# Optimization experiments

Measured on AMD Instinct MI355X. Metric: run time of the kernel, lower is better.

The kernel has to match this reference:

```python
import jax, jax.numpy as jnp
import numpy as np
import math

B, N, D, KA, H = 8, 1024, 512, 16, 8
QD = D // 4
HD = D // H


def qsplit(x):
    q = x.shape[-1] // 4
    return x[..., :q], x[..., q:2*q], x[..., 2*q:3*q], x[..., 3*q:]


def hprod(p, q):
    pr, pi, pj, pk = qsplit(p)
    qr, qi, qj, qk = qsplit(q)
    return jnp.concatenate([
        pr*qr - pi*qi - pj*qj - pk*qk,
        pr*qi + pi*qr + pj*qk - pk*qj,
        pr*qj - pi*qk + pj*qr + pk*qi,
        pr*qk + pi*qj - pj*qi + pk*qr,
    ], axis=-1)


def qconj(x):
    r, i, j, k = qsplit(x)
    return jnp.concatenate([r, -i, -j, -k], axis=-1)


def qlin(x, w, b):
    # w: [4, qo, qi] -> Hamilton block matrix [4qo, 4qi]
    r, i, j, k = w[0], w[1], w[2], w[3]
    W = jnp.concatenate([
        jnp.concatenate([r, -i, -j, -k], axis=1),
        jnp.concatenate([i,  r, -k,  j], axis=1),
        jnp.concatenate([j,  k,  r, -i], axis=1),
        jnp.concatenate([k, -j,  i,  r], axis=1),
    ], axis=0)
    return x @ W.T + b


def qln(x, gamma, beta):
    # per-component LayerNorm over Q; gamma/beta: [4, Q]
    qd = x.shape[-1] // 4
    xs = x.reshape(x.shape[:-1] + (4, qd))
    m = xs.mean(-1, keepdims=True)
    v = xs.var(-1, keepdims=True)
    y = (xs - m) / jnp.sqrt(v + 1e-5) * gamma + beta
    return y.reshape(x.shape)


def setup_inputs():
    key = jax.random.key(0)
    ks = jax.random.split(key, 20)
    lim = math.sqrt(6.0 / (2 * QD))  # xavier for [QD, QD]
    def qw(k):
        return jax.random.uniform(k, (4, QD, QD), minval=-lim, maxval=lim)
    return {
        'q': jax.random.normal(ks[0], (B, N, D), dtype=jnp.float32),
        'spike': jax.random.uniform(ks[1], (B, N), dtype=jnp.float32),
        'mask': jnp.ones((B, N), dtype=jnp.float32),
        'theta_logit': jnp.float32(0.0),
        'w_prim': qw(ks[2]), 'b_prim': jnp.zeros((D,), jnp.float32),
        'anchors': jax.random.normal(ks[3], (KA, D)) * 0.5,
        'log_sigma': jnp.zeros((KA,), jnp.float32),
        'w_aggr': qw(ks[4]), 'b_aggr': jnp.zeros((D,), jnp.float32),
        'w_q': qw(ks[5]), 'b_q': jnp.zeros((D,), jnp.float32),
        'w_k': qw(ks[6]), 'b_k': jnp.zeros((D,), jnp.float32),
        'w_v': qw(ks[7]), 'b_v': jnp.zeros((D,), jnp.float32),
        'w_o': qw(ks[8]), 'b_o': jnp.zeros((D,), jnp.float32),
        'ln_gamma': jnp.ones((4, QD), jnp.float32),
        'ln_beta': jnp.zeros((4, QD), jnp.float32),
    }


def reference(q, spike, mask, theta_logit, w_prim, b_prim, anchors, log_sigma,
              w_aggr, b_aggr, w_q, b_q, w_k, b_k, w_v, b_v, w_o, b_o,
              ln_gamma, ln_beta):
    b, n, d = q.shape
    qd = d // 4
    # --- SpikeQuaternionRotation: rotate toward K-axis by theta = theta_max*spike ---
    theta_max = (jnp.pi / 2) * jax.nn.sigmoid(theta_logit)
    theta = theta_max * spike                      # [B, N]
    c = jnp.cos(theta)[..., None]
    s = jnp.sin(theta)[..., None]
    z = jnp.zeros_like(c)
    rot = jnp.concatenate([
        jnp.broadcast_to(c, (b, n, qd)),
        jnp.broadcast_to(z, (b, n, qd)),
        jnp.broadcast_to(z, (b, n, qd)),
        jnp.broadcast_to(s, (b, n, qd)),
    ], axis=-1)
    q_rot = hprod(rot, q)                          # [B, N, D]

    # --- PrimaryLayer: per-cell quaternion transform ---
    msg_p = qlin(q_rot, w_prim, b_prim)

    # --- QuaternionAnchorLayer ---
    a_conj = qconj(anchors)                        # [KA, D]
    prod = hprod(q_rot[:, None, :, :], a_conj[None, :, None, :])  # [B, KA, N, D]
    dist = jnp.sum(prod * prod, axis=-1)           # [B, KA, N]
    sigma_sq = jnp.maximum(jnp.exp(log_sigma) ** 2, 1e-6)
    incid = jnp.exp(-dist / sigma_sq[None, :, None]) * mask[:, None, :]
    denom = jnp.maximum(incid.sum(-1, keepdims=True), 1e-6)
    h = jnp.einsum('bkn,bnd->bkd', incid, q_rot) / denom  # [B, KA, D]
    h = qlin(h, w_aggr, b_aggr)

    # --- QuaternionMHA(query=q_rot, key=h, value=h), no mask ---
    Qh = qlin(q_rot, w_q, b_q).reshape(b, n, H, HD)
    Kh = qlin(h, w_k, b_k).reshape(b, KA, H, HD)
    Vh = qlin(h, w_v, b_v).reshape(b, KA, H, HD)
    scores = jnp.einsum('bqhd,bkhd->bhqk', Qh, Kh) / jnp.sqrt(jnp.float32(HD))
    attn = jax.nn.softmax(scores, axis=-1)
    out = jnp.einsum('bhqk,bkhd->bqhd', attn, Vh).reshape(b, n, d)
    msg_a = qlin(out, w_o, b_o)

    # --- residual + per-component LayerNorm ---
    return qln(q + msg_p + msg_a, ln_gamma, ln_beta)
```

## Files before the change

kernel.cpp:

```cpp
#include <hip/hip_runtime.h>
#include <hip/hip_bf16.h>

typedef __hip_bfloat16 bf16;
typedef __attribute__((ext_vector_type(8))) short bf16x8;
typedef __attribute__((ext_vector_type(4))) float f32x4;

__device__ __forceinline__ float bflo(unsigned u) { return __uint_as_float(u << 16); }
__device__ __forceinline__ float bfhi(unsigned u) { return __uint_as_float(u & 0xffff0000u); }
__device__ __forceinline__ bool probe_f32(const void* mask) {
  return *(const unsigned*)mask == 0x3F800000u;
}
__device__ __forceinline__ float ldin(const void* p, size_t i, bool f32) {
  return f32 ? ((const float*)p)[i] : (float)((const bf16*)p)[i];
}


__global__ __launch_bounds__(256) void prologue(
    const void* w0, const void* w1, const void* w2, const void* w3,
    const void* w4, const void* w5,
    const void* b0, const void* b1, const void* b2, const void* b3,
    const void* b4, const void* b5, const void* g_, const void* be,
    const void* q, const void* spike, const void* theta_logit, const void* mask,
    bf16* __restrict__ Wall, float* __restrict__ biasF,
    bf16* __restrict__ q_rot, float* __restrict__ qn) {
  bool f32 = probe_f32(mask);
  int blk = blockIdx.x, t = threadIdx.x;
  if (blk < 1536) {
    int E = blk * 1024 + t * 4;
    int g = E >> 9;
    int wi = g >> 9;
    int o = g & 511;
    int k0 = E & 511;
    const void* src = wi == 0 ? w0 : wi == 1 ? w1 : wi == 2 ? w2 : wi == 3 ? w3 : wi == 4 ? w4 : w5;
    int ro = o >> 7, a = o & 127, co = k0 >> 7;
    int comp = ro ^ co;
    float sgn = ((0x284Eu >> (ro * 4 + co)) & 1u) ? -1.0f : 1.0f;
    bf16 ov[4];
    #pragma unroll
    for (int j = 0; j < 4; ++j) {
      int b2 = (k0 & 127) + j;
      ov[j] = (bf16)(ldin(src, comp * 16384 + a * 128 + b2, f32) * sgn);
    }
    int r = g & 63, c = k0 >> 3;
    size_t off = (size_t)(g >> 6) * 65536 + (size_t)((c >> 2) * 4096 + (r >> 4) * 1024
               + ((c & 3) * 16 + (r & 15)) * 16 + (k0 & 7) * 2);
    *(uint2*)((char*)Wall + off) = *(const uint2*)ov;
  } else if (blk < 1544) {
    int b = blk - 1536;
    const void* src = b == 0 ? b0 : b == 1 ? b1 : b == 2 ? b2 : b == 3 ? b3
                    : b == 4 ? b4 : b == 5 ? b5 : b == 6 ? g_ : be;
    biasF[b * 512 + t] = ldin(src, t, f32);
    biasF[b * 512 + 256 + t] = ldin(src, 256 + t, f32);
  } else {
    int row = (blk - 1544) * 2 + (t >> 7);
    int l = t & 127;
    float tl = ldin(theta_logit, 0, f32);
    float tmax = 1.5707963267948966f / (1.0f + __expf(-tl));
    float th = tmax * ldin(spike, row, f32);
    float c = cosf(th), s = sinf(th);
    size_t base = (size_t)row * 512;
    float a = ldin(q, base + l, f32), b = ldin(q, base + 128 + l, f32);
    float cc = ldin(q, base + 256 + l, f32), d = ldin(q, base + 384 + l, f32);
    float r0 = c * a - s * d;
    float r1 = c * b - s * cc;
    float r2 = c * cc + s * b;
    float r3 = c * d + s * a;
    bf16* orow = q_rot + base;
    orow[l] = (bf16)r0; orow[128 + l] = (bf16)r1; orow[256 + l] = (bf16)r2; orow[384 + l] = (bf16)r3;
    qn[(size_t)row * 128 + l] = r0 * r0 + r1 * r1 + r2 * r2 + r3 * r3;
  }
}

__device__ __forceinline__ void stage_B64(const bf16* __restrict__ Bw, int n0, char* Bs, int t) {
  const char* src = (const char*)Bw + (size_t)(n0 >> 6) * 65536;
  #pragma unroll
  for (int i = 0; i < 16; ++i)
    *(uint4*)(Bs + t * 16 + i * 4096) = *(const uint4*)(src + t * 16 + i * 4096);
}

__global__ __launch_bounds__(256, 2) void gemm_dist(
    const bf16* __restrict__ A, const bf16* __restrict__ Bw,
    const float* __restrict__ bias0, const float* __restrict__ bias1,
    bf16* __restrict__ MQ,
    const float* __restrict__ qn, const void* anchors, const void* lsig,
    const void* mask, float* __restrict__ h_part, float* __restrict__ pd_part) {
  __shared__ char smem[77952];
  const int t = threadIdx.x;
  if (blockIdx.x >= 128) {
    char* Bs = smem;
    const int g = blockIdx.x - 128;
    const int wave = t >> 6, lane = t & 63;
    const int quad = lane >> 4, l16 = lane & 15;
    const int m0 = (g & 31) * 256, n0 = (g >> 5) * 64;
    stage_B64(Bw, n0, Bs, t);
    __syncthreads();
    const int mbase = m0 + wave * 64;
    f32x4 acc[4][4] = {};
    bf16x8 areg[2][4], breg[2][4];
    #pragma unroll
    for (int mt = 0; mt < 4; ++mt)
      areg[0][mt] = *(const bf16x8*)(A + (size_t)(mbase + mt * 16 + l16) * 512 + quad * 8);
    #pragma unroll
    for (int nt = 0; nt < 4; ++nt)
      breg[0][nt] = *(const bf16x8*)(Bs + nt * 1024 + lane * 16);
    #pragma unroll
    for (int kk = 0; kk < 16; ++kk) {
      const int cur = kk & 1, nxt = cur ^ 1;
      if (kk < 15) {
        const int k2 = (kk + 1) * 32;
        #pragma unroll
        for (int mt = 0; mt < 4; ++mt)
          areg[nxt][mt] = *(const bf16x8*)(A + (size_t)(mbase + mt * 16 + l16) * 512 + k2 + quad * 8);
        #pragma unroll
        for (int nt = 0; nt < 4; ++nt)
          breg[nxt][nt] = *(const bf16x8*)(Bs + (kk + 1) * 4096 + nt * 1024 + lane * 16);
      }
      #pragma unroll
      for (int mt = 0; mt < 4; ++mt)
        #pragma unroll
        for (int nt = 0; nt < 4; ++nt)
          acc[mt][nt] = __builtin_amdgcn_mfma_f32_16x16x32_bf16(areg[cur][mt], breg[cur][nt],
                                                                acc[mt][nt], 0, 0, 0);
    }
    #pragma unroll
    for (int nt = 0; nt < 4; ++nt) {
      int col = n0 + nt * 16 + l16;
      float bv = col < 512 ? bias0[col] : bias1[col - 512];
      #pragma unroll
      for (int mt = 0; mt < 4; ++mt) {
        int rb = mbase + mt * 16 + quad * 4;
        #pragma unroll
        for (int r = 0; r < 4; ++r)
          MQ[(size_t)(rb + r) * 1024 + col] = (bf16)(acc[mt][nt][r] + bv);
      }
    }
  } else {
    bool f32 = probe_f32(mask);
    bf16*  qr    = (bf16*)smem;
    float* an    = (float*)(smem + 65536);
    float* sIncT = (float*)(smem + 73728);
    float* rs    = (float*)(smem + 77824);
    float* pd    = (float*)(smem + 77888);
    int bb = blockIdx.x;
    int b = bb >> 4, nc = bb & 15;
    {
      const uint4* src = (const uint4*)((const bf16*)A + ((size_t)b * 1024 + nc * 64) * 512);
      uint4* dst = (uint4*)qr;
      #pragma unroll
      for (int i = 0; i < 16; ++i) dst[t + i * 256] = src[t + i * 256];
    }
    for (int i = t; i < 2048; i += 256) {
      int k = i >> 7, l = i & 127;
      float a0 = ldin(anchors, k * 512 + l, f32);
      float a1 = ldin(anchors, k * 512 + 128 + l, f32);
      float a2 = ldin(anchors, k * 512 + 256 + l, f32);
      float a3 = ldin(anchors, k * 512 + 384 + l, f32);
      an[i] = a0 * a0 + a1 * a1 + a2 * a2 + a3 * a3;
    }
    if (t < 16) {
      float ls = ldin(lsig, t, f32);
      float ssq = __expf(ls); ssq = fmaxf(ssq * ssq, 1e-6f);
      rs[t] = -1.0f / ssq;
      pd[t] = 0.0f;
    }
    __syncthreads();
    {
      int rl = t >> 2, part = t & 3;
      int n = nc * 64 + rl;
      const float* qrow = qn + ((size_t)b * 1024 + n) * 128 + part * 32;
      f32x4 q4[8];
      #pragma unroll
      for (int i = 0; i < 8; ++i) q4[i] = *(const f32x4*)(qrow + i * 4);
      float sc[16] = {};
      #pragma unroll
      for (int i = 0; i < 8; ++i) {
        #pragma unroll
        for (int k = 0; k < 16; ++k) {
          f32x4 av = *(const f32x4*)(an + k * 128 + part * 32 + i * 4);
          sc[k] += q4[i][0] * av[0] + q4[i][1] * av[1] + q4[i][2] * av[2] + q4[i][3] * av[3];
        }
      }
      #pragma unroll
      for (int k = 0; k < 16; ++k) {
        sc[k] += __shfl_xor(sc[k], 1, 64);
        sc[k] += __shfl_xor(sc[k], 2, 64);
      }
      if (part == 0) {
        float mval = ldin(mask, b * 1024 + n, f32);
        #pragma unroll
        for (int k = 0; k < 16; ++k) {
          float inc = __expf(sc[k] * rs[k]) * mval;
          sIncT[rl * 16 + k] = inc;
          atomicAdd(&pd[k], inc);
        }
      }
    }
    __syncthreads();
    {
      float acc0[16] = {}, acc1[16] = {};
      for (int nn = 0; nn < 64; ++nn) {
        unsigned u = *(const unsigned*)(qr + nn * 512 + 2 * t);
        float v0 = bflo(u);
        float v1 = bfhi(u);
        f32x4 p0 = *(const f32x4*)(sIncT + nn * 16);
        f32x4 p1 = *(const f32x4*)(sIncT + nn * 16 + 4);
        f32x4 p2 = *(const f32x4*)(sIncT + nn * 16 + 8);
        f32x4 p3 = *(const f32x4*)(sIncT + nn * 16 + 12);
        #pragma unroll
        for (int j = 0; j < 4; ++j) {
          acc0[j]      += p0[j] * v0; acc1[j]      += p0[j] * v1;
          acc0[4 + j]  += p1[j] * v0; acc1[4 + j]  += p1[j] * v1;
          acc0[8 + j]  += p2[j] * v0; acc1[8 + j]  += p2[j] * v1;
          acc0[12 + j] += p3[j] * v0; acc1[12 + j] += p3[j] * v1;
        }
      }
      #pragma unroll
      for (int k = 0; k < 16; ++k) {
        size_t base = ((size_t)(b * 16 + k) * 16 + nc) * 512;
        float2 o2 = {acc0[k], acc1[k]};
        *(float2*)(h_part + base + 2 * t) = o2;
      }
    }
    if (t < 16) pd_part[((size_t)(b * 16 + t)) * 16 + nc] = pd[t];
  }
}

__device__ __forceinline__ float dotW4(const char* WallB, int gRow, const float* xp512, int c4lo) {
  const char* p = WallB + (size_t)(gRow >> 6) * 65536
                + (size_t)(((gRow >> 4) & 3) * 1024 + (gRow & 15) * 16);
  float acc = 0.0f;
  #pragma unroll
  for (int c4 = c4lo; c4 < c4lo + 4; ++c4) {
    #pragma unroll
    for (int cl = 0; cl < 4; ++cl) {
      uint4 u = *(const uint4*)(p + c4 * 4096 + cl * 256);
      const float* xp = xp512 + c4 * 32 + cl * 8;
      acc += xp[0] * bflo(u.x) + xp[1] * bfhi(u.x)
           + xp[2] * bflo(u.y) + xp[3] * bfhi(u.y)
           + xp[4] * bflo(u.z) + xp[5] * bfhi(u.z)
           + xp[6] * bflo(u.w) + xp[7] * bfhi(u.w);
    }
  }
  return acc;
}

__global__ __launch_bounds__(256) void aggr_k(
    const float* __restrict__ h_part, const float* __restrict__ pd_part,
    const bf16* __restrict__ Wall, const float* __restrict__ biasF,
    float* __restrict__ h_aggr) {
  __shared__ float xs[512];
  const char* WallB = (const char*)Wall;
  const float* ba = biasF + 1536;
  const int gy = blockIdx.x >> 7, row = blockIdx.x & 127;
  const int t = threadIdx.x;
  float dsum = 0.0f;
  #pragma unroll
  for (int nc = 0; nc < 16; ++nc) dsum += pd_part[row * 16 + nc];
  float dinv = 1.0f / fmaxf(dsum, 1e-6f);
  #pragma unroll
  for (int j = 0; j < 2; ++j) {
    int d = j * 256 + t;
    float hv = 0.0f;
    #pragma unroll
    for (int nc = 0; nc < 16; ++nc) hv += h_part[(size_t)row * 8192 + nc * 512 + d];
    xs[d] = hv * dinv;
  }
  __syncthreads();
  const int o = gy * 64 + (t >> 2), part = t & 3;
  float acc = dotW4(WallB, 1536 + o, xs, part * 4);
  acc += __shfl_xor(acc, 1, 64);
  acc += __shfl_xor(acc, 2, 64);
  if (part == 0) h_aggr[(size_t)row * 512 + o] = acc + ba[o];
}

__global__ __launch_bounds__(256) void kv_k(
    const float* __restrict__ h_aggr, const bf16* __restrict__ Wall,
    const float* __restrict__ biasF,
    float* __restrict__ Kh, float* __restrict__ Vh) {
  __shared__ float ys[512];
  const char* WallB = (const char*)Wall;
  const float* bk = biasF + 2048;
  const float* bv = biasF + 2560;
  const int gy = blockIdx.x >> 7, row = blockIdx.x & 127;
  const int t = threadIdx.x;
  #pragma unroll
  for (int j = 0; j < 2; ++j) {
    int d = j * 256 + t;
    ys[d] = h_aggr[(size_t)row * 512 + d];
  }
  __syncthreads();
  const int o = gy * 64 + (t >> 2), part = t & 3;
  float ak = dotW4(WallB, 2048 + o, ys, part * 4);
  float av = dotW4(WallB, 2560 + o, ys, part * 4);
  ak += __shfl_xor(ak, 1, 64);
  ak += __shfl_xor(ak, 2, 64);
  av += __shfl_xor(av, 1, 64);
  av += __shfl_xor(av, 2, 64);
  if (part == 0) {
    Kh[(size_t)row * 512 + o] = ak + bk[o];
    Vh[(size_t)row * 512 + o] = av + bv[o];
  }
}

__global__ __launch_bounds__(256, 2) void attn_tail(
    const bf16* __restrict__ MQ, const float* __restrict__ Kh_g,
    const float* __restrict__ Vh_g, const bf16* __restrict__ Wall,
    const float* __restrict__ biasF, const void* q, const void* mask, void* out) {
  __shared__ float KV[8 * 1092];
  __shared__ float P[16 * 132];
  const bool f32 = probe_f32(mask);
  const int t = threadIdx.x;
  const int rowbase = blockIdx.x * 16;
  const int b = rowbase >> 10;
  for (int i = t; i < 8192; i += 256) {
    int k = i >> 9, d = i & 511, h = d >> 6, dd = d & 63;
    KV[h * 1092 + k * 68 + dd] = Kh_g[(size_t)b * 8192 + i];
  }
  __syncthreads();
  {
    const int r = t >> 4, h = (t >> 1) & 7, hf = t & 1;
    const int grow = rowbase + r;
    const uint4* qp = (const uint4*)(MQ + (size_t)grow * 1024 + 512 + h * 64 + hf * 32);
    float qv[32];
    #pragma unroll
    for (int i = 0; i < 4; ++i) {
      uint4 u = qp[i];
      qv[i * 8 + 0] = bflo(u.x); qv[i * 8 + 1] = bfhi(u.x);
      qv[i * 8 + 2] = bflo(u.y); qv[i * 8 + 3] = bfhi(u.y);
      qv[i * 8 + 4] = bflo(u.z); qv[i * 8 + 5] = bfhi(u.z);
      qv[i * 8 + 6] = bflo(u.w); qv[i * 8 + 7] = bfhi(u.w);
    }
    float sc[16];
    #pragma unroll
    for (int k = 0; k < 16; ++k) {
      float s = 0.0f;
      #pragma unroll
      for (int d4 = 0; d4 < 8; ++d4) {
        f32x4 kv = *(const f32x4*)(KV + h * 1092 + k * 68 + hf * 32 + d4 * 4);
        s += qv[d4 * 4 + 0] * kv[0] + qv[d4 * 4 + 1] * kv[1]
           + qv[d4 * 4 + 2] * kv[2] + qv[d4 * 4 + 3] * kv[3];
      }
      sc[k] = s;
    }
    #pragma unroll
    for (int k = 0; k < 16; ++k) sc[k] += __shfl_xor(sc[k], 1, 64);
    if (hf == 0) {
      #pragma unroll
      for (int k = 0; k < 16; ++k) sc[k] *= 0.125f;
      float m = sc[0];
      #pragma unroll
      for (int k = 1; k < 16; ++k) m = fmaxf(m, sc[k]);
      float ssum = 0.0f;
      #pragma unroll
      for (int k = 0; k < 16; ++k) { sc[k] = __expf(sc[k] - m); ssum += sc[k]; }
      float inv = 1.0f / ssum;
      #pragma unroll
      for (int k = 0; k < 16; ++k) P[r * 132 + h * 16 + k] = sc[k] * inv;
    }
  }
  __syncthreads();
  for (int i = t; i < 8192; i += 256) {
    int k = i >> 9, d = i & 511, h = d >> 6, dd = d & 63;
    KV[h * 1092 + k * 68 + dd] = Vh_g[(size_t)b * 8192 + i];
  }
  __syncthreads();
  float pv[8][4];
  {
    const int r = t >> 4, dg = t & 15;
    #pragma unroll
    for (int h = 0; h < 8; ++h) {
      float a0 = 0, a1 = 0, a2 = 0, a3 = 0;
      #pragma unroll
      for (int k = 0; k < 16; ++k) {
        float p = P[r * 132 + h * 16 + k];
        f32x4 va = *(const f32x4*)(KV + h * 1092 + k * 68 + dg * 4);
        a0 += p * va[0]; a1 += p * va[1]; a2 += p * va[2]; a3 += p * va[3];
      }
      pv[h][0] = a0; pv[h][1] = a1; pv[h][2] = a2; pv[h][3] = a3;
    }
  }
  __syncthreads();
  char* A_lds = (char*)KV;
  {
    const int r = t >> 4, dg = t & 15;
    #pragma unroll
    for (int h = 0; h < 8; ++h) {
      int c0 = h * 64 + dg * 4;
      int off = (c0 >> 5) * 1024 + ((c0 >> 3) & 3) * 256 + r * 16 + (c0 & 7) * 2;
      bf16 ov[4] = {(bf16)pv[h][0], (bf16)pv[h][1], (bf16)pv[h][2], (bf16)pv[h][3]};
      *(uint2*)(A_lds + off) = *(const uint2*)ov;
    }
  }
  __syncthreads();
  const int wave = t >> 6, lane = t & 63, quad = lane >> 4, l16 = lane & 15;
  const char* WallB = (const char*)Wall;
  f32x4 acc[8] = {};
  bf16x8 breg[2][8];
  bf16x8 areg[2];
  areg[0] = *(const bf16x8*)(A_lds + quad * 256 + l16 * 16);
  #pragma unroll
  for (int nt = 0; nt < 8; ++nt) {
    size_t cb = (size_t)(16 + wave * 2 + (nt >> 2)) * 65536;
    breg[0][nt] = *(const bf16x8*)(WallB + cb + (nt & 3) * 1024 + lane * 16);
  }
  #pragma unroll
  for (int kk = 0; kk < 16; ++kk) {
    const int cur = kk & 1, nxt = cur ^ 1;
    if (kk < 15) {
      areg[nxt] = *(const bf16x8*)(A_lds + (kk + 1) * 1024 + quad * 256 + l16 * 16);
      #pragma unroll
      for (int nt = 0; nt < 8; ++nt) {
        size_t cb = (size_t)(16 + wave * 2 + (nt >> 2)) * 65536;
        breg[nxt][nt] = *(const bf16x8*)(WallB + cb + (kk + 1) * 4096 + (nt & 3) * 1024 + lane * 16);
      }
    }
    #pragma unroll
    for (int nt = 0; nt < 8; ++nt)
      acc[nt] = __builtin_amdgcn_mfma_f32_16x16x32_bf16(areg[cur], breg[cur][nt], acc[nt], 0, 0, 0);
  }
  const float* biasO = biasF + 1024;
  const float* gamF = biasF + 3072;
  float xv[8][4];
  float s[4] = {0, 0, 0, 0}, s2[4] = {0, 0, 0, 0};
  #pragma unroll
  for (int nt = 0; nt < 8; ++nt) {
    int gcol = wave * 128 + nt * 16 + l16;
    float bo = biasO[gcol];
    #pragma unroll
    for (int reg = 0; reg < 4; ++reg) {
      int grow = rowbase + quad * 4 + reg;
      float qv = ldin(q, (size_t)grow * 512 + gcol, f32);
      float mp = (float)MQ[(size_t)grow * 1024 + gcol];
      float x = qv + mp + acc[nt][reg] + bo;
      xv[nt][reg] = x;
      s[reg] += x; s2[reg] += x * x;
    }
  }
  #pragma unroll
  for (int reg = 0; reg < 4; ++reg) {
    #pragma unroll
    for (int off = 1; off <= 8; off <<= 1) {
      s[reg]  += __shfl_xor(s[reg], off, 64);
      s2[reg] += __shfl_xor(s2[reg], off, 64);
    }
  }
  #pragma unroll
  for (int reg = 0; reg < 4; ++reg) {
    float m = s[reg] * (1.0f / 128.0f);
    float rinv = rsqrtf(s2[reg] * (1.0f / 128.0f) - m * m + 1e-5f);
    int grow = rowbase + quad * 4 + reg;
    #pragma unroll
    for (int nt = 0; nt < 8; ++nt) {
      int gcol = wave * 128 + nt * 16 + l16;
      float y = (xv[nt][reg] - m) * rinv * gamF[gcol] + gamF[512 + gcol];
      if (f32) ((float*)out)[(size_t)grow * 512 + gcol] = y;
      else     ((bf16*)out)[(size_t)grow * 512 + gcol] = (bf16)y;
    }
  }
}

extern "C" void kernel_launch(void* const* d_in, const int* in_sizes, int n_in,
                              void* d_out, int out_size, void* d_ws, size_t ws_size,
                              hipStream_t stream) {
  (void)in_sizes; (void)n_in; (void)out_size; (void)ws_size;
  const void* q      = d_in[0];
  const void* spike  = d_in[1];
  const void* mask   = d_in[2];
  const void* tl     = d_in[3];
  const void* w_prim = d_in[4];
  const void* b_prim = d_in[5];
  const void* anchors= d_in[6];
  const void* lsig   = d_in[7];
  const void* w_aggr = d_in[8];
  const void* b_aggr = d_in[9];
  const void* w_q    = d_in[10];
  const void* b_q    = d_in[11];
  const void* w_k    = d_in[12];
  const void* b_k    = d_in[13];
  const void* w_v    = d_in[14];
  const void* b_v    = d_in[15];
  const void* w_o    = d_in[16];
  const void* b_o    = d_in[17];
  const void* gam    = d_in[18];
  const void* bet    = d_in[19];

  char* ws = (char*)d_ws;
  bf16*  Wall   = (bf16*)(ws + 0);
  bf16*  q_rot  = (bf16*)(ws + 3145728);
  float* qn     = (float*)(ws + 11534336);
  bf16*  MQ     = (bf16*)(ws + 15728640);
  float* h_part = (float*)(ws + 32505856);
  float* pd_part= (float*)(ws + 36700160);
  float* Kh     = (float*)(ws + 36708352);
  float* Vh     = (float*)(ws + 36970496);
  float* biasF  = (float*)(ws + 37232640);
  float* h_aggr = (float*)(ws + 37249024);

  prologue<<<5640, 256, 0, stream>>>(w_prim, w_q, w_o, w_aggr, w_k, w_v,
                                     b_prim, b_q, b_o, b_aggr, b_k, b_v, gam, bet,
                                     q, spike, tl, mask, Wall, biasF, q_rot, qn);
  gemm_dist<<<640, 256, 0, stream>>>(q_rot, Wall, biasF + 0, biasF + 512, MQ,
                                     qn, anchors, lsig, mask, h_part, pd_part);
  aggr_k<<<1024, 256, 0, stream>>>(h_part, pd_part, Wall, biasF, h_aggr);
  kv_k<<<1024, 256, 0, stream>>>(h_aggr, Wall, biasF, Kh, Vh);
  attn_tail<<<512, 256, 0, stream>>>(MQ, Kh, Vh, Wall, biasF, q, mask, d_out);
}
```

Baseline: 189.0 us.

## Fuse aggregation and K/V projections into one kernel; widen attention tail tiles

Merges aggr_k and kv_k into a single 1024-thread kernel per (batch, anchor) row that keeps h_aggr in shared memory, removing one launch and a global round trip. The attention tail now processes 32 rows per block instead of 16, with one thread per (row, head) and two MFMA M-tiles per wave, so K/V staging and weight loads are amortized over twice the rows. In exchange the fused kernel runs only 128 blocks, leaving much of the GPU idle and re-reading the weights per row, and the tail uses more registers and launches half as many blocks.

```diff
diff --git a/kernel.cpp b/kernel.cpp
--- a/kernel.cpp
+++ b/kernel.cpp
@@ -225,12 +225,12 @@
   }
 }
 
-__device__ __forceinline__ float dotW4(const char* WallB, int gRow, const float* xp512, int c4lo) {
+__device__ __forceinline__ float dotW8(const char* WallB, int gRow, const float* xp512, int c4lo) {
   const char* p = WallB + (size_t)(gRow >> 6) * 65536
                 + (size_t)(((gRow >> 4) & 3) * 1024 + (gRow & 15) * 16);
   float acc = 0.0f;
   #pragma unroll
-  for (int c4 = c4lo; c4 < c4lo + 4; ++c4) {
+  for (int c4 = c4lo; c4 < c4lo + 8; ++c4) {
     #pragma unroll
     for (int cl = 0; cl < 4; ++cl) {
       uint4 u = *(const uint4*)(p + c4 * 4096 + cl * 256);
@@ -244,61 +244,45 @@
   return acc;
 }
 
-__global__ __launch_bounds__(256) void aggr_k(
+__global__ __launch_bounds__(1024) void akv_k(
     const float* __restrict__ h_part, const float* __restrict__ pd_part,
     const bf16* __restrict__ Wall, const float* __restrict__ biasF,
-    float* __restrict__ h_aggr) {
+    float* __restrict__ Kh, float* __restrict__ Vh) {
   __shared__ float xs[512];
+  __shared__ float ys[512];
   const char* WallB = (const char*)Wall;
   const float* ba = biasF + 1536;
-  const int gy = blockIdx.x >> 7, row = blockIdx.x & 127;
+  const float* bk = biasF + 2048;
+  const float* bv = biasF + 2560;
+  const int row = blockIdx.x;
   const int t = threadIdx.x;
   float dsum = 0.0f;
   #pragma unroll
   for (int nc = 0; nc < 16; ++nc) dsum += pd_part[row * 16 + nc];
   float dinv = 1.0f / fmaxf(dsum, 1e-6f);
-  #pragma unroll
-  for (int j = 0; j < 2; ++j) {
-    int d = j * 256 + t;
+  if (t < 512) {
     float hv = 0.0f;
     #pragma unroll
-    for (int nc = 0; nc < 16; ++nc) hv += h_part[(size_t)row * 8192 + nc * 512 + d];
-    xs[d] = hv * dinv;
-  }
-  __syncthreads();
-  const int o = gy * 64 + (t >> 2), part = t & 3;
-  float acc = dotW4(WallB, 1536 + o, xs, part * 4);
-  acc += __shfl_xor(acc, 1, 64);
-  acc += __shfl_xor(acc, 2, 64);
-  if (part == 0) h_aggr[(size_t)row * 512 + o] = acc + ba[o];
-}
-
-__global__ __launch_bounds__(256) void kv_k(
-    const float* __restrict__ h_aggr, const bf16* __restrict__ Wall,
-    const float* __restrict__ biasF,
-    float* __restrict__ Kh, float* __restrict__ Vh) {
-  __shared__ float ys[512];
-  const char* WallB = (const char*)Wall;
-  const float* bk = biasF + 2048;
-  const float* bv = biasF + 2560;
-  const int gy = blockIdx.x >> 7, row = blockIdx.x & 127;
-  const int t = threadIdx.x;
-  #pragma unroll
-  for (int j = 0; j < 2; ++j) {
-    int d = j * 256 + t;
-    ys[d] = h_aggr[(size_t)row * 512 + d];
-  }
-  __syncthreads();
-  const int o = gy * 64 + (t >> 2), part = t & 3;
-  float ak = dotW4(WallB, 2048 + o, ys, part * 4);
-  float av = dotW4(WallB, 2560 + o, ys, part * 4);
-  ak += __shfl_xor(ak, 1, 64);
-  ak += __shfl_xor(ak, 2, 64);
-  av += __shfl_xor(av, 1, 64);
-  av += __shfl_xor(av, 2, 64);
-  if (part == 0) {
-    Kh[(size_t)row * 512 + o] = ak + bk[o];
-    Vh[(size_t)row * 512 + o] = av + bv[o];
+    for (int nc = 0; nc < 16; ++nc) hv += h_part[(size_t)row * 8192 + nc * 512 + t];
+    xs[t] = hv * dinv;
+  }
+  __syncthreads();
+  const int o = t >> 1, part = t & 1;
+  {
+    float acc = dotW8(WallB, 1536 + o, xs, part * 8);
+    acc += __shfl_xor(acc, 1, 64);
+    if (part == 0) ys[o] = acc + ba[o];
+  }
+  __syncthreads();
+  {
+    float ak = dotW8(WallB, 2048 + o, ys, part * 8);
+    float av = dotW8(WallB, 2560 + o, ys, part * 8);
+    ak += __shfl_xor(ak, 1, 64);
+    av += __shfl_xor(av, 1, 64);
+    if (part == 0) {
+      Kh[(size_t)row * 512 + o] = ak + bk[o];
+      Vh[(size_t)row * 512 + o] = av + bv[o];
+    }
   }
 }
 
@@ -307,10 +291,10 @@
     const float* __restrict__ Vh_g, const bf16* __restrict__ Wall,
     const float* __restrict__ biasF, const void* q, const void* mask, void* out) {
   __shared__ float KV[8 * 1092];
-  __shared__ float P[16 * 132];
+  __shared__ float P[32 * 132];
   const bool f32 = probe_f32(mask);
   const int t = threadIdx.x;
-  const int rowbase = blockIdx.x * 16;
+  const int rowbase = blockIdx.x * 32;
   const int b = rowbase >> 10;
   for (int i = t; i < 8192; i += 256) {
     int k = i >> 9, d = i & 511, h = d >> 6, dd = d & 63;
@@ -318,45 +302,42 @@
   }
   __syncthreads();
   {
-    const int r = t >> 4, h = (t >> 1) & 7, hf = t & 1;
+    const int r = t >> 3, h = t & 7;
     const int grow = rowbase + r;
-    const uint4* qp = (const uint4*)(MQ + (size_t)grow * 1024 + 512 + h * 64 + hf * 32);
-    float qv[32];
-    #pragma unroll
-    for (int i = 0; i < 4; ++i) {
-      uint4 u = qp[i];
-      qv[i * 8 + 0] = bflo(u.x); qv[i * 8 + 1] = bfhi(u.x);
-      qv[i * 8 + 2] = bflo(u.y); qv[i * 8 + 3] = bfhi(u.y);
-      qv[i * 8 + 4] = bflo(u.z); qv[i * 8 + 5] = bfhi(u.z);
-      qv[i * 8 + 6] = bflo(u.w); qv[i * 8 + 7] = bfhi(u.w);
-    }
-    float sc[16];
-    #pragma unroll
-    for (int k = 0; k < 16; ++k) {
-      float s = 0.0f;
-      #pragma unroll
-      for (int d4 = 0; d4 < 8; ++d4) {
-        f32x4 kv = *(const f32x4*)(KV + h * 1092 + k * 68 + hf * 32 + d4 * 4);
-        s += qv[d4 * 4 + 0] * kv[0] + qv[d4 * 4 + 1] * kv[1]
-           + qv[d4 * 4 + 2] * kv[2] + qv[d4 * 4 + 3] * kv[3];
-      }
-      sc[k] = s;
-    }
-    #pragma unroll
-    for (int k = 0; k < 16; ++k) sc[k] += __shfl_xor(sc[k], 1, 64);
-    if (hf == 0) {
-      #pragma unroll
-      for (int k = 0; k < 16; ++k) sc[k] *= 0.125f;
-      float m = sc[0];
-      #pragma unroll
-      for (int k = 1; k < 16; ++k) m = fmaxf(m, sc[k]);
-      float ssum = 0.0f;
-      #pragma unroll
-      for (int k = 0; k < 16; ++k) { sc[k] = __expf(sc[k] - m); ssum += sc[k]; }
-      float inv = 1.0f / ssum;
-      #pragma unroll
-      for (int k = 0; k < 16; ++k) P[r * 132 + h * 16 + k] = sc[k] * inv;
-    }
+    const uint4* qp = (const uint4*)(MQ + (size_t)grow * 1024 + 512 + h * 64);
+    float sc[16] = {};
+    #pragma unroll
+    for (int c = 0; c < 4; ++c) {
+      uint4 u0 = qp[c * 2], u1 = qp[c * 2 + 1];
+      float qv[16];
+      qv[0] = bflo(u0.x); qv[1] = bfhi(u0.x); qv[2] = bflo(u0.y); qv[3] = bfhi(u0.y);
+      qv[4] = bflo(u0.z); qv[5] = bfhi(u0.z); qv[6] = bflo(u0.w); qv[7] = bfhi(u0.w);
+      qv[8] = bflo(u1.x); qv[9] = bfhi(u1.x); qv[10] = bflo(u1.y); qv[11] = bfhi(u1.y);
+      qv[12] = bflo(u1.z); qv[13] = bfhi(u1.z); qv[14] = bflo(u1.w); qv[15] = bfhi(u1.w);
+      #pragma unroll
+      for (int k = 0; k < 16; ++k) {
+        const float* kp = KV + h * 1092 + k * 68 + c * 16;
+        f32x4 k0 = *(const f32x4*)(kp);
+        f32x4 k1 = *(const f32x4*)(kp + 4);
+        f32x4 k2 = *(const f32x4*)(kp + 8);
+        f32x4 k3 = *(const f32x4*)(kp + 12);
+        sc[k] += qv[0] * k0[0] + qv[1] * k0[1] + qv[2] * k0[2] + qv[3] * k0[3]
+               + qv[4] * k1[0] + qv[5] * k1[1] + qv[6] * k1[2] + qv[7] * k1[3]
+               + qv[8] * k2[0] + qv[9] * k2[1] + qv[10] * k2[2] + qv[11] * k2[3]
+               + qv[12] * k3[0] + qv[13] * k3[1] + qv[14] * k3[2] + qv[15] * k3[3];
+      }
+    }
+    #pragma unroll
+    for (int k = 0; k < 16; ++k) sc[k] *= 0.125f;
+    float m = sc[0];
+    #pragma unroll
+    for (int k = 1; k < 16; ++k) m = fmaxf(m, sc[k]);
+    float ssum = 0.0f;
+    #pragma unroll
+    for (int k = 0; k < 16; ++k) { sc[k] = __expf(sc[k] - m); ssum += sc[k]; }
+    float inv = 1.0f / ssum;
+    #pragma unroll
+    for (int k = 0; k < 16; ++k) P[r * 132 + h * 16 + k] = sc[k] * inv;
   }
   __syncthreads();
   for (int i = t; i < 8192; i += 256) {
@@ -364,40 +345,48 @@
     KV[h * 1092 + k * 68 + dd] = Vh_g[(size_t)b * 8192 + i];
   }
   __syncthreads();
-  float pv[8][4];
+  float pv[8][8];
   {
-    const int r = t >> 4, dg = t & 15;
+    const int r = t >> 3, dg = t & 7;
     #pragma unroll
     for (int h = 0; h < 8; ++h) {
-      float a0 = 0, a1 = 0, a2 = 0, a3 = 0;
+      float a0 = 0, a1 = 0, a2 = 0, a3 = 0, a4 = 0, a5 = 0, a6 = 0, a7 = 0;
       #pragma unroll
       for (int k = 0; k < 16; ++k) {
         float p = P[r * 132 + h * 16 + k];
-        f32x4 va = *(const f32x4*)(KV + h * 1092 + k * 68 + dg * 4);
-        a0 += p * va[0]; a1 += p * va[1]; a2 += p * va[2]; a3 += p * va[3];
+        const float* vp = KV + h * 1092 + k * 68 + dg * 8;
+        f32x4 v0 = *(const f32x4*)vp;
+        f32x4 v1 = *(const f32x4*)(vp + 4);
+        a0 += p * v0[0]; a1 += p * v0[1]; a2 += p * v0[2]; a3 += p * v0[3];
+        a4 += p * v1[0]; a5 += p * v1[1]; a6 += p * v1[2]; a7 += p * v1[3];
       }
       pv[h][0] = a0; pv[h][1] = a1; pv[h][2] = a2; pv[h][3] = a3;
+      pv[h][4] = a4; pv[h][5] = a5; pv[h][6] = a6; pv[h][7] = a7;
     }
   }
   __syncthreads();
   char* A_lds = (char*)KV;
   {
-    const int r = t >> 4, dg = t & 15;
+    const int r = t >> 3, dg = t & 7;
     #pragma unroll
     for (int h = 0; h < 8; ++h) {
-      int c0 = h * 64 + dg * 4;
-      int off = (c0 >> 5) * 1024 + ((c0 >> 3) & 3) * 256 + r * 16 + (c0 & 7) * 2;
-      bf16 ov[4] = {(bf16)pv[h][0], (bf16)pv[h][1], (bf16)pv[h][2], (bf16)pv[h][3]};
-      *(uint2*)(A_lds + off) = *(const uint2*)ov;
+      int c = h * 8 + dg;
+      int off = (c >> 2) * 2048 + (r >> 4) * 1024 + ((c & 3) * 16 + (r & 15)) * 16;
+      bf16 ov[8];
+      #pragma unroll
+      for (int j = 0; j < 8; ++j) ov[j] = (bf16)pv[h][j];
+      *(uint4*)(A_lds + off) = *(const uint4*)ov;
     }
   }
   __syncthreads();
   const int wave = t >> 6, lane = t & 63, quad = lane >> 4, l16 = lane & 15;
   const char* WallB = (const char*)Wall;
-  f32x4 acc[8] = {};
+  f32x4 acc[2][8] = {};
   bf16x8 breg[2][8];
-  bf16x8 areg[2];
-  areg[0] = *(const bf16x8*)(A_lds + quad * 256 + l16 * 16);
+  bf16x8 areg[2][2];
+  #pragma unroll
+  for (int mt = 0; mt < 2; ++mt)
+    areg[0][mt] = *(const bf16x8*)(A_lds + mt * 1024 + lane * 16);
   #pragma unroll
   for (int nt = 0; nt < 8; ++nt) {
     size_t cb = (size_t)(16 + wave * 2 + (nt >> 2)) * 65536;
@@ -407,7 +396,9 @@
   for (int kk = 0; kk < 16; ++kk) {
     const int cur = kk & 1, nxt = cur ^ 1;
     if (kk < 15) {
-      areg[nxt] = *(const bf16x8*)(A_lds + (kk + 1) * 1024 + quad * 256 + l16 * 16);
+      #pragma unroll
+      for (int mt = 0; mt < 2; ++mt)
+        areg[nxt][mt] = *(const bf16x8*)(A_lds + (kk + 1) * 2048 + mt * 1024 + lane * 16);
       #pragma unroll
       for (int nt = 0; nt < 8; ++nt) {
         size_t cb = (size_t)(16 + wave * 2 + (nt >> 2)) * 65536;
@@ -415,48 +406,56 @@
       }
     }
     #pragma unroll
-    for (int nt = 0; nt < 8; ++nt)
-      acc[nt] = __builtin_amdgcn_mfma_f32_16x16x32_bf16(areg[cur], breg[cur][nt], acc[nt], 0, 0, 0);
+    for (int mt = 0; mt < 2; ++mt)
+      #pragma unroll
+      for (int nt = 0; nt < 8; ++nt)
+        acc[mt][nt] = __builtin_amdgcn_mfma_f32_16x16x32_bf16(areg[cur][mt], breg[cur][nt],
+                                                              acc[mt][nt], 0, 0, 0);
   }
   const float* biasO = biasF + 1024;
   const float* gamF = biasF + 3072;
-  float xv[8][4];
-  float s[4] = {0, 0, 0, 0}, s2[4] = {0, 0, 0, 0};
-  #pragma unroll
-  for (int nt = 0; nt < 8; ++nt) {
-    int gcol = wave * 128 + nt * 16 + l16;
-    float bo = biasO[gcol];
-    #pragma unroll
-    for (int reg = 0; reg < 4; ++reg) {
-      int grow = rowbase + quad * 4 + reg;
-      float qv = ldin(q, (size_t)grow * 512 + gcol, f32);
-      float mp = (float)MQ[(size_t)grow * 1024 + gcol];
-      float x = qv + mp + acc[nt][reg] + bo;
-      xv[nt][reg] = x;
-      s[reg] += x; s2[reg] += x * x;
-    }
-  }
-  #pragma unroll
-  for (int reg = 0; reg < 4; ++reg) {
-    #pragma unroll
-    for (int off = 1; off <= 8; off <<= 1) {
-      s[reg]  += __shfl_xor(s[reg], off, 64);
-      s2[reg] += __shfl_xor(s2[reg], off, 64);
-    }
-  }
-  #pragma unroll
-  for (int reg = 0; reg < 4; ++reg) {
-    float m = s[reg] * (1.0f / 128.0f);
-    float rinv = rsqrtf(s2[reg] * (1.0f / 128.0f) - m * m + 1e-5f);
-    int grow = rowbase + quad * 4 + reg;
+  float s[2][4] = {}, s2[2][4] = {};
+  #pragma unroll
+  for (int mt = 0; mt < 2; ++mt)
     #pragma unroll
     for (int nt = 0; nt < 8; ++nt) {
       int gcol = wave * 128 + nt * 16 + l16;
-      float y = (xv[nt][reg] - m) * rinv * gamF[gcol] + gamF[512 + gcol];
-      if (f32) ((float*)out)[(size_t)grow * 512 + gcol] = y;
-      else     ((bf16*)out)[(size_t)grow * 512 + gcol] = (bf16)y;
-    }
-  }
+      float bo = biasO[gcol];
+      #pragma unroll
+      for (int reg = 0; reg < 4; ++reg) {
+        int grow = rowbase + mt * 16 + quad * 4 + reg;
+        float qv = ldin(q, (size_t)grow * 512 + gcol, f32);
+        float mp = (float)MQ[(size_t)grow * 1024 + gcol];
+        float x = qv + mp + acc[mt][nt][reg] + bo;
+        acc[mt][nt][reg] = x;
+        s[mt][reg] += x; s2[mt][reg] += x * x;
+      }
+    }
+  #pragma unroll
+  for (int mt = 0; mt < 2; ++mt)
+    #pragma unroll
+    for (int reg = 0; reg < 4; ++reg) {
+      #pragma unroll
+      for (int off = 1; off <= 8; off <<= 1) {
+        s[mt][reg]  += __shfl_xor(s[mt][reg], off, 64);
+        s2[mt][reg] += __shfl_xor(s2[mt][reg], off, 64);
+      }
+    }
+  #pragma unroll
+  for (int mt = 0; mt < 2; ++mt)
+    #pragma unroll
+    for (int reg = 0; reg < 4; ++reg) {
+      float m = s[mt][reg] * (1.0f / 128.0f);
+      float rinv = rsqrtf(s2[mt][reg] * (1.0f / 128.0f) - m * m + 1e-5f);
+      int grow = rowbase + mt * 16 + quad * 4 + reg;
+      #pragma unroll
+      for (int nt = 0; nt < 8; ++nt) {
+        int gcol = wave * 128 + nt * 16 + l16;
+        float y = (acc[mt][nt][reg] - m) * rinv * gamF[gcol] + gamF[512 + gcol];
+        if (f32) ((float*)out)[(size_t)grow * 512 + gcol] = y;
+        else     ((bf16*)out)[(size_t)grow * 512 + gcol] = (bf16)y;
+      }
+    }
 }
 
 extern "C" void kernel_launch(void* const* d_in, const int* in_sizes, int n_in,
@@ -494,14 +493,12 @@
   float* Kh     = (float*)(ws + 36708352);
   float* Vh     = (float*)(ws + 36970496);
   float* biasF  = (float*)(ws + 37232640);
-  float* h_aggr = (float*)(ws + 37249024);
 
   prologue<<<5640, 256, 0, stream>>>(w_prim, w_q, w_o, w_aggr, w_k, w_v,
                                      b_prim, b_q, b_o, b_aggr, b_k, b_v, gam, bet,
                                      q, spike, tl, mask, Wall, biasF, q_rot, qn);
   gemm_dist<<<640, 256, 0, stream>>>(q_rot, Wall, biasF + 0, biasF + 512, MQ,
                                      qn, anchors, lsig, mask, h_part, pd_part);
-  aggr_k<<<1024, 256, 0, stream>>>(h_part, pd_part, Wall, biasF, h_aggr);
-  kv_k<<<1024, 256, 0, stream>>>(h_aggr, Wall, biasF, Kh, Vh);
-  attn_tail<<<512, 256, 0, stream>>>(MQ, Kh, Vh, Wall, biasF, q, mask, d_out);
-}
+  akv_k<<<128, 1024, 0, stream>>>(h_part, pd_part, Wall, biasF, Kh, Vh);
+  attn_tail<<<256, 256, 0, stream>>>(MQ, Kh, Vh, Wall, biasF, q, mask, d_out);
+}
```

Result: slower. 208.2 us (+10.1%).
